# Kernel tuning notes

Measured on AMD Instinct MI355X. Metric: run time of the kernel, lower is better.

The kernel has to match this reference:

```python
import jax, jax.numpy as jnp
import numpy as np

H = 16            # L-BFGS history length
N = 4_000_000     # number of parameters
HIGH = jax.lax.Precision.HIGHEST


def setup_inputs() -> dict:
    key = jax.random.key(0)
    k1, k2, k3 = jax.random.split(key, 3)
    # Small-scale steps so inner products are well conditioned.
    y = jax.random.normal(k1, (H, N), jnp.float32) * 0.01           # S_k: parameter diffs
    g = y + 0.1 * jax.random.normal(k2, (H, N), jnp.float32) * 0.01  # Y_k: grad diffs, s_i.g_i > 0
    pytree = jax.random.normal(k3, (N,), jnp.float32)
    sy = jnp.dot(y, g.T, precision=HIGH)                 # [H,H] s_i . y_j
    cross = jnp.tril(sy, k=-1)                           # L_k (strictly lower triangular)
    diag = jnp.diag(sy)                                  # diag(D_k), positive by construction
    s_inner = jnp.dot(y, y.T, precision=HIGH)            # S^T S
    return {
        "pytree": pytree,
        "y_diff_history": y,
        "grad_diff_history": g,
        "y_diff_grad_diff_cross_inner": cross,
        "y_diff_grad_diff_inner": diag,
        "y_diff_cross_inner": s_inner,
        "index_start": 21,  # > H: buffer full, circular-roll branch active
    }


def reference(pytree, y_diff_history, grad_diff_history,
              y_diff_grad_diff_cross_inner, y_diff_grad_diff_inner,
              y_diff_cross_inner, index_start):
    h = y_diff_history.shape[0]
    idx = (index_start - 1) % h
    s_last = y_diff_history[idx]
    g_last = grad_diff_history[idx]
    curvature = jnp.dot(s_last, g_last, precision=HIGH)
    gamma = jnp.where(curvature > 0,
                      jnp.dot(g_last, g_last, precision=HIGH) / curvature,
                      jnp.float32(1.0))
    d = jnp.where(y_diff_grad_diff_inner == 0, 1.0, y_diff_grad_diff_inner)
    L = y_diff_grad_diff_cross_inner
    # J J^T = gamma * S^T S + L D^-1 L^T
    J_square = gamma * y_diff_cross_inner + jnp.dot(L / d, L.T, precision=HIGH)
    J = jnp.linalg.cholesky(J_square)
    # Project input onto the two history bases: [2H]
    top = jnp.einsum('hn,n->h', grad_diff_history, pytree, precision=HIGH)
    bot = gamma * jnp.einsum('hn,n->h', y_diff_history, pytree, precision=HIGH)
    descent = jnp.concatenate([top, bot])
    roll_by = -(index_start % h)

    def maybe_roll(v, r):
        return jax.lax.cond(index_start <= h, lambda x: x, lambda x: jnp.roll(x, r), v)

    descent = descent.at[:h].set(maybe_roll(descent[:h], roll_by))
    descent = descent.at[h:].set(maybe_roll(descent[h:], roll_by))
    sqrt_d = jnp.sqrt(d)
    low_tri = jnp.block([
        [jnp.diag(sqrt_d), jnp.zeros((h, h), descent.dtype)],
        [-L / sqrt_d, J],
    ])
    descent = jax.scipy.linalg.solve_triangular(low_tri, descent, lower=True)
    upper_tri = low_tri.T
    upper_tri = upper_tri.at[:h].set(-upper_tri[:h])
    descent = jax.scipy.linalg.solve_triangular(upper_tri, descent, lower=False)
    descent = descent.at[:h].set(maybe_roll(descent[:h], -roll_by))
    descent = descent.at[h:].set(maybe_roll(descent[h:], -roll_by))
    out = (gamma * pytree
           - jnp.einsum('h,hn->n', descent[:h], grad_diff_history, precision=HIGH)
           - gamma * jnp.einsum('h,hn->n', descent[h:], y_diff_history, precision=HIGH))
    return out
```

## Files before the change

### kernel.cpp

```cpp
#include <hip/hip_runtime.h>

#define HH 16
#define RED_VALS 34
#define OUTBLK 2048
#define RBLK 977

__global__ __launch_bounds__(256) void lbfgs_reduce_line(
    const float* __restrict__ p, const float* __restrict__ y,
    const float* __restrict__ g, const int* __restrict__ idxp,
    float* __restrict__ partials, int nblk, int n) {
  const int nchunk = n >> 2;
  const int is = idxp[0];
  const int hidx = ((is - 1) % HH + HH) % HH;
  const int K = (nchunk + (gridDim.x << 8) - 1) / (gridDim.x << 8);

  float accg[HH], accy[HH];
#pragma unroll
  for (int i = 0; i < HH; ++i) { accg[i] = 0.f; accy[i] = 0.f; }
  float ac = 0.f, agg = 0.f;

  for (int k = 0; k < K; ++k) {
    const int c = (blockIdx.x + k * gridDim.x) * 256 + threadIdx.x;
    if (c < nchunk) {
      const float4 pv = reinterpret_cast<const float4*>(p)[c];
      float4 gv[HH], yv[HH];
#pragma unroll
      for (int i = 0; i < HH; ++i)
        gv[i] = reinterpret_cast<const float4*>(g + (size_t)i * n)[c];
#pragma unroll
      for (int i = 0; i < HH; ++i)
        yv[i] = reinterpret_cast<const float4*>(y + (size_t)i * n)[c];
      __builtin_amdgcn_sched_barrier(0);
#pragma unroll
      for (int i = 0; i < HH; ++i) {
        accg[i] += gv[i].x * pv.x + gv[i].y * pv.y + gv[i].z * pv.z + gv[i].w * pv.w;
        accy[i] += yv[i].x * pv.x + yv[i].y * pv.y + yv[i].z * pv.z + yv[i].w * pv.w;
        float dyg = yv[i].x * gv[i].x + yv[i].y * gv[i].y +
                    yv[i].z * gv[i].z + yv[i].w * gv[i].w;
        float dgg = gv[i].x * gv[i].x + gv[i].y * gv[i].y +
                    gv[i].z * gv[i].z + gv[i].w * gv[i].w;
        ac  += (i == hidx) ? dyg : 0.f;
        agg += (i == hidx) ? dgg : 0.f;
      }
    }
  }
  if (blockIdx.x == 0) {
    for (int e = (nchunk << 2) + threadIdx.x; e < n; e += 256) {
      float pv = p[e];
#pragma unroll
      for (int i = 0; i < HH; ++i) {
        float gs = g[(size_t)i * n + e], ys = y[(size_t)i * n + e];
        accg[i] += gs * pv;
        accy[i] += ys * pv;
        ac  += (i == hidx) ? ys * gs : 0.f;
        agg += (i == hidx) ? gs * gs : 0.f;
      }
    }
  }

  __shared__ float red[4][RED_VALS];
  const int wave = threadIdx.x >> 6, lane = threadIdx.x & 63;
#pragma unroll
  for (int i = 0; i < HH; ++i) {
    float v = accg[i];
#pragma unroll
    for (int off = 32; off > 0; off >>= 1) v += __shfl_down(v, off);
    if (lane == 0) red[wave][i] = v;
    float w = accy[i];
#pragma unroll
    for (int off = 32; off > 0; off >>= 1) w += __shfl_down(w, off);
    if (lane == 0) red[wave][HH + i] = w;
  }
  {
    float v = ac;
#pragma unroll
    for (int off = 32; off > 0; off >>= 1) v += __shfl_down(v, off);
    if (lane == 0) red[wave][32] = v;
    float w = agg;
#pragma unroll
    for (int off = 32; off > 0; off >>= 1) w += __shfl_down(w, off);
    if (lane == 0) red[wave][33] = w;
  }
  __syncthreads();
  if (threadIdx.x < RED_VALS) {
    float s = red[0][threadIdx.x] + red[1][threadIdx.x] +
              red[2][threadIdx.x] + red[3][threadIdx.x];
    partials[(size_t)threadIdx.x * nblk + blockIdx.x] = s;
  }
}

__global__ __launch_bounds__(256) void lbfgs_stage2(
    const float* __restrict__ partials, int nblk, float* __restrict__ sums) {
  const int j = blockIdx.x;
  float v = 0.f;
  for (int b = threadIdx.x; b < nblk; b += 256)
    v += partials[(size_t)j * nblk + b];
#pragma unroll
  for (int off = 32; off > 0; off >>= 1) v += __shfl_down(v, off);
  __shared__ float red[4];
  const int wave = threadIdx.x >> 6, lane = threadIdx.x & 63;
  if (lane == 0) red[wave] = v;
  __syncthreads();
  if (threadIdx.x == 0)
    sums[j] = red[0] + red[1] + red[2] + red[3];
}

__global__ __launch_bounds__(256) void lbfgs_solve(
    const float* __restrict__ sums_g,
    const float* __restrict__ Lmat, const float* __restrict__ diag,
    const float* __restrict__ sinner, const int* __restrict__ idxp,
    float* __restrict__ coeff) {
  __shared__ float sums[RED_VALS];
  if (threadIdx.x < RED_VALS) sums[threadIdx.x] = sums_g[threadIdx.x];
  __syncthreads();

  __shared__ float Lsh[HH][HH];
  __shared__ float dd[HH], sqd[HH];
  __shared__ float Jsq[HH][HH];
  __shared__ float gamma_s;
  __shared__ float x[2 * HH];
  {
    int i = threadIdx.x >> 4, j = threadIdx.x & 15;
    if (threadIdx.x < 256) Lsh[i][j] = Lmat[i * HH + j];
  }
  if (threadIdx.x < HH) {
    float dv = diag[threadIdx.x];
    float ddv = (dv == 0.f) ? 1.f : dv;
    dd[threadIdx.x] = ddv;
    sqd[threadIdx.x] = sqrtf(ddv);
  }
  if (threadIdx.x == 0) {
    float cur = sums[32], gg = sums[33];
    gamma_s = (cur > 0.f) ? (gg / cur) : 1.f;
  }
  __syncthreads();
  {
    int i = threadIdx.x >> 4, j = threadIdx.x & 15;
    float v = gamma_s * sinner[i * HH + j];
#pragma unroll
    for (int k = 0; k < HH; ++k) v += Lsh[i][k] * Lsh[j][k] / dd[k];
    Jsq[i][j] = v;
  }
  __syncthreads();
  if (threadIdx.x == 0) {
    for (int c = 0; c < HH; ++c) {
      float s = Jsq[c][c];
      for (int k = 0; k < c; ++k) s -= Jsq[c][k] * Jsq[c][k];
      float dv = sqrtf(s);
      Jsq[c][c] = dv;
      float inv = 1.f / dv;
      for (int r = c + 1; r < HH; ++r) {
        float s2 = Jsq[r][c];
        for (int k = 0; k < c; ++k) s2 -= Jsq[r][k] * Jsq[c][k];
        Jsq[r][c] = s2 * inv;
      }
    }
    const int is = idxp[0];
    const int sh = (is <= HH) ? 0 : (is % HH);
    const float gamma = gamma_s;
    for (int k = 0; k < HH; ++k) {
      x[k]      = sums[(k + sh) & (HH - 1)];
      x[HH + k] = gamma * sums[HH + ((k + sh) & (HH - 1))];
    }
    for (int i = 0; i < HH; ++i) x[i] /= sqd[i];
    for (int i = 0; i < HH; ++i) {
      float s = x[HH + i];
      for (int j = 0; j < HH; ++j) s += (Lsh[i][j] / sqd[j]) * x[j];
      for (int j = 0; j < i; ++j) s -= Jsq[i][j] * x[HH + j];
      x[HH + i] = s / Jsq[i][i];
    }
    for (int i = HH - 1; i >= 0; --i) {
      float s = x[HH + i];
      for (int j = i + 1; j < HH; ++j) s -= Jsq[j][i] * x[HH + j];
      x[HH + i] = s / Jsq[i][i];
    }
    for (int i = 0; i < HH; ++i) {
      float s = x[i];
      for (int j = 0; j < HH; ++j) s -= (Lsh[j][i] / sqd[i]) * x[HH + j];
      x[i] = s / (-sqd[i]);
    }
    coeff[0] = gamma;
    for (int k = 0; k < HH; ++k) {
      coeff[1 + k]      = x[(k - sh + HH) & (HH - 1)];
      coeff[1 + HH + k] = gamma * x[HH + ((k - sh + HH) & (HH - 1))];
    }
  }
}

__global__ __launch_bounds__(256) void lbfgs_output(
    const float* __restrict__ p, const float* __restrict__ y,
    const float* __restrict__ g, const float* __restrict__ coeff,
    float* __restrict__ out, int n) {
  const float gamma = coeff[0];
  float a[HH], b[HH];
#pragma unroll
  for (int i = 0; i < HH; ++i) {
    a[i] = coeff[1 + i];
    b[i] = coeff[1 + HH + i];
  }
  const int tid = blockIdx.x * blockDim.x + threadIdx.x;
  const int nth = gridDim.x * blockDim.x;
  const int nchunk = n >> 2;
  const float4* __restrict__ p4 = reinterpret_cast<const float4*>(p);
  float4* __restrict__ out4 = reinterpret_cast<float4*>(out);
  for (int c = tid; c < nchunk; c += nth) {
    float4 pv = p4[c];
    float ox = gamma * pv.x, oy = gamma * pv.y;
    float oz = gamma * pv.z, ow = gamma * pv.w;
#pragma unroll
    for (int i = 0; i < HH; ++i) {
      const float4 gv = reinterpret_cast<const float4*>(g + (size_t)i * n)[c];
      const float4 yv = reinterpret_cast<const float4*>(y + (size_t)i * n)[c];
      ox -= a[i] * gv.x + b[i] * yv.x;
      oy -= a[i] * gv.y + b[i] * yv.y;
      oz -= a[i] * gv.z + b[i] * yv.z;
      ow -= a[i] * gv.w + b[i] * yv.w;
    }
    out4[c] = make_float4(ox, oy, oz, ow);
  }
  for (int c = (nchunk << 2) + tid; c < n; c += nth) {
    float pv = p[c];
    float o = gamma * pv;
#pragma unroll
    for (int i = 0; i < HH; ++i)
      o -= a[i] * g[(size_t)i * n + c] + b[i] * y[(size_t)i * n + c];
    out[c] = o;
  }
}

extern "C" void kernel_launch(void* const* d_in, const int* in_sizes, int n_in,
                              void* d_out, int out_size, void* d_ws, size_t ws_size,
                              hipStream_t stream) {
  const float* p      = (const float*)d_in[0];
  const float* y      = (const float*)d_in[1];
  const float* g      = (const float*)d_in[2];
  const float* Lmat   = (const float*)d_in[3];
  const float* diag   = (const float*)d_in[4];
  const float* sinner = (const float*)d_in[5];
  const int*   idxp   = (const int*)d_in[6];
  float* out = (float*)d_out;
  float* wsf = (float*)d_ws;
  const int n = in_sizes[0];

  int nblk = RBLK;
  {
    long avail = (long)(ws_size / sizeof(float)) - RED_VALS - 64;
    long cap = avail / RED_VALS;
    if (cap < nblk) nblk = (int)(cap < 1 ? 1 : cap);
  }
  float* partials = wsf;
  float* sums     = wsf + (size_t)RED_VALS * nblk;
  float* coeff    = sums + RED_VALS;

  lbfgs_reduce_line<<<dim3(nblk), dim3(256), 0, stream>>>(
      p, y, g, idxp, partials, nblk, n);
  lbfgs_stage2<<<dim3(RED_VALS), dim3(256), 0, stream>>>(partials, nblk, sums);
  lbfgs_solve<<<dim3(1), dim3(256), 0, stream>>>(sums, Lmat, diag,
                                                 sinner, idxp, coeff);
  lbfgs_output<<<dim3(OUTBLK), dim3(256), 0, stream>>>(p, y, g, coeff, out, n);
}
```

Before: 232.5 us.

## Split reduction into one-wave-per-row dot products over a 2D grid

The fused reduction kernel is replaced. Before, each thread loaded p plus all 32 history rows and kept 34 accumulators. Now a 2D grid assigns one wave per history row (or per curvature dot product), and each wave handles a single 64-chunk slice. This is meant to cut register pressure and raise occupancy and memory-level parallelism. In exchange, p and the hidx row are re-read once per row, which adds cache traffic. There are also far more, very short waves, and the partial buffer grows to 15625 entries per value, so the second-stage reduction has much more to sum.

```diff
diff --git a/kernel.cpp b/kernel.cpp
--- a/kernel.cpp
+++ b/kernel.cpp
@@ -3,90 +3,57 @@
 #define HH 16
 #define RED_VALS 34
 #define OUTBLK 2048
-#define RBLK 977
-
-__global__ __launch_bounds__(256) void lbfgs_reduce_line(
+
+__global__ __launch_bounds__(256) void lbfgs_reduce_tlp(
     const float* __restrict__ p, const float* __restrict__ y,
     const float* __restrict__ g, const int* __restrict__ idxp,
-    float* __restrict__ partials, int nblk, int n) {
+    float* __restrict__ partials, int ngrp, int n) {
+  const int grp = blockIdx.x;
+  const int wave = threadIdx.x >> 6, lane = threadIdx.x & 63;
   const int nchunk = n >> 2;
   const int is = idxp[0];
   const int hidx = ((is - 1) % HH + HH) % HH;
-  const int K = (nchunk + (gridDim.x << 8) - 1) / (gridDim.x << 8);
-
-  float accg[HH], accy[HH];
-#pragma unroll
-  for (int i = 0; i < HH; ++i) { accg[i] = 0.f; accy[i] = 0.f; }
-  float ac = 0.f, agg = 0.f;
-
-  for (int k = 0; k < K; ++k) {
-    const int c = (blockIdx.x + k * gridDim.x) * 256 + threadIdx.x;
-    if (c < nchunk) {
-      const float4 pv = reinterpret_cast<const float4*>(p)[c];
-      float4 gv[HH], yv[HH];
-#pragma unroll
-      for (int i = 0; i < HH; ++i)
-        gv[i] = reinterpret_cast<const float4*>(g + (size_t)i * n)[c];
-#pragma unroll
-      for (int i = 0; i < HH; ++i)
-        yv[i] = reinterpret_cast<const float4*>(y + (size_t)i * n)[c];
-      __builtin_amdgcn_sched_barrier(0);
-#pragma unroll
-      for (int i = 0; i < HH; ++i) {
-        accg[i] += gv[i].x * pv.x + gv[i].y * pv.y + gv[i].z * pv.z + gv[i].w * pv.w;
-        accy[i] += yv[i].x * pv.x + yv[i].y * pv.y + yv[i].z * pv.z + yv[i].w * pv.w;
-        float dyg = yv[i].x * gv[i].x + yv[i].y * gv[i].y +
-                    yv[i].z * gv[i].z + yv[i].w * gv[i].w;
-        float dgg = gv[i].x * gv[i].x + gv[i].y * gv[i].y +
-                    gv[i].z * gv[i].z + gv[i].w * gv[i].w;
-        ac  += (i == hidx) ? dyg : 0.f;
-        agg += (i == hidx) ? dgg : 0.f;
-      }
-    }
-  }
-  if (blockIdx.x == 0) {
-    for (int e = (nchunk << 2) + threadIdx.x; e < n; e += 256) {
-      float pv = p[e];
-#pragma unroll
-      for (int i = 0; i < HH; ++i) {
-        float gs = g[(size_t)i * n + e], ys = y[(size_t)i * n + e];
-        accg[i] += gs * pv;
-        accy[i] += ys * pv;
-        ac  += (i == hidx) ? ys * gs : 0.f;
-        agg += (i == hidx) ? gs * gs : 0.f;
-      }
-    }
-  }
-
-  __shared__ float red[4][RED_VALS];
-  const int wave = threadIdx.x >> 6, lane = threadIdx.x & 63;
-#pragma unroll
-  for (int i = 0; i < HH; ++i) {
-    float v = accg[i];
-#pragma unroll
-    for (int off = 32; off > 0; off >>= 1) v += __shfl_down(v, off);
-    if (lane == 0) red[wave][i] = v;
-    float w = accy[i];
-#pragma unroll
-    for (int off = 32; off > 0; off >>= 1) w += __shfl_down(w, off);
-    if (lane == 0) red[wave][HH + i] = w;
-  }
-  {
-    float v = ac;
-#pragma unroll
-    for (int off = 32; off > 0; off >>= 1) v += __shfl_down(v, off);
-    if (lane == 0) red[wave][32] = v;
-    float w = agg;
-#pragma unroll
-    for (int off = 32; off > 0; off >>= 1) w += __shfl_down(w, off);
-    if (lane == 0) red[wave][33] = w;
-  }
-  __syncthreads();
-  if (threadIdx.x < RED_VALS) {
-    float s = red[0][threadIdx.x] + red[1][threadIdx.x] +
-              red[2][threadIdx.x] + red[3][threadIdx.x];
-    partials[(size_t)threadIdx.x * nblk + blockIdx.x] = s;
-  }
+
+  float v = 0.f;
+  int outj = -1;
+
+  if (blockIdx.y < 8) {
+    const int r = blockIdx.y * 4 + wave;
+    const float* __restrict__ row =
+        (r < HH) ? (g + (size_t)r * n) : (y + (size_t)(r - HH) * n);
+    const float4* __restrict__ row4 = reinterpret_cast<const float4*>(row);
+    const float4* __restrict__ p4 = reinterpret_cast<const float4*>(p);
+    for (int c = grp * 64 + lane; c < nchunk; c += ngrp * 64) {
+      float4 rv = row4[c];
+      float4 pv = p4[c];
+      v += rv.x * pv.x + rv.y * pv.y + rv.z * pv.z + rv.w * pv.w;
+    }
+    if (grp == 0) {
+      for (int e = (nchunk << 2) + lane; e < n; e += 64)
+        v += row[e] * p[e];
+    }
+    outj = r;
+  } else if (wave < 2) {
+    const float* __restrict__ gh = g + (size_t)hidx * n;
+    const float* __restrict__ oth = (wave == 0) ? (y + (size_t)hidx * n) : gh;
+    const float4* __restrict__ gh4 = reinterpret_cast<const float4*>(gh);
+    const float4* __restrict__ ot4 = reinterpret_cast<const float4*>(oth);
+    for (int c = grp * 64 + lane; c < nchunk; c += ngrp * 64) {
+      float4 a = gh4[c];
+      float4 b = ot4[c];
+      v += a.x * b.x + a.y * b.y + a.z * b.z + a.w * b.w;
+    }
+    if (grp == 0) {
+      for (int e = (nchunk << 2) + lane; e < n; e += 64)
+        v += gh[e] * oth[e];
+    }
+    outj = 32 + wave;
+  }
+
+#pragma unroll
+  for (int off = 32; off > 0; off >>= 1) v += __shfl_down(v, off);
+  if (lane == 0 && outj >= 0)
+    partials[(size_t)outj * ngrp + grp] = v;
 }
 
 __global__ __launch_bounds__(256) void lbfgs_stage2(
@@ -242,19 +209,21 @@
   float* wsf = (float*)d_ws;
   const int n = in_sizes[0];
 
-  int nblk = RBLK;
+  const int nchunk = n >> 2;
+  int ngrp = (nchunk + 63) / 64;
   {
     long avail = (long)(ws_size / sizeof(float)) - RED_VALS - 64;
     long cap = avail / RED_VALS;
-    if (cap < nblk) nblk = (int)(cap < 1 ? 1 : cap);
+    if (cap < 1) cap = 1;
+    if (ngrp > cap) ngrp = (int)cap;
   }
   float* partials = wsf;
-  float* sums     = wsf + (size_t)RED_VALS * nblk;
+  float* sums     = wsf + (size_t)RED_VALS * ngrp;
   float* coeff    = sums + RED_VALS;
 
-  lbfgs_reduce_line<<<dim3(nblk), dim3(256), 0, stream>>>(
-      p, y, g, idxp, partials, nblk, n);
-  lbfgs_stage2<<<dim3(RED_VALS), dim3(256), 0, stream>>>(partials, nblk, sums);
+  lbfgs_reduce_tlp<<<dim3(ngrp, 9), dim3(256), 0, stream>>>(
+      p, y, g, idxp, partials, ngrp, n);
+  lbfgs_stage2<<<dim3(RED_VALS), dim3(256), 0, stream>>>(partials, ngrp, sums);
   lbfgs_solve<<<dim3(1), dim3(256), 0, stream>>>(sums, Lmat, diag,
                                                  sinner, idxp, coeff);
   lbfgs_output<<<dim3(OUTBLK), dim3(256), 0, stream>>>(p, y, g, coeff, out, n);
```

Result: slower. 272.9 us (+17.4%).
